# Performance work log

Measured on AMD Instinct MI355X. Metric: run time of the kernel, lower is better.

Reference implementation:

```python
import jax, jax.numpy as jnp
import numpy as np
import math

EPS = 1e-12


def _cmul(ar, ai, br, bi):
    return ar * br - ai * bi, ar * bi + ai * br


def _wilson_seed(x):
    # x: (B, 4, L, L) -> conj of canonical Wilson-line path, (B, L, L) re/im
    ux_r, ux_i, uy_r, uy_i = x[:, 0], x[:, 1], x[:, 2], x[:, 3]
    B, L, _ = ux_r.shape
    dt = x.dtype

    def step(c, u):
        cr, ci = c
        ur, ui = u
        nr, ni = _cmul(cr, ci, ur, ui)
        return (nr, ni), (nr, ni)

    # cumulative complex product along x at y=0
    init_r = jnp.ones((B,), dt)
    init_i = jnp.zeros((B,), dt)
    xs = (ux_r[:, :-1, 0].T, ux_i[:, :-1, 0].T)  # (L-1, B)
    _, (axr, axi) = jax.lax.scan(step, (init_r, init_i), xs)
    x_axis_r = jnp.concatenate([init_r[None], axr], 0).T  # (B, L)
    x_axis_i = jnp.concatenate([init_i[None], axi], 0).T

    # cumulative complex product along y, vectorized over x
    ys = (jnp.moveaxis(uy_r[:, :, :-1], 2, 0), jnp.moveaxis(uy_i[:, :, :-1], 2, 0))  # (L-1, B, L)
    _, (pr, pi_) = jax.lax.scan(step, (x_axis_r, x_axis_i), ys)
    path_r = jnp.moveaxis(jnp.concatenate([x_axis_r[None], pr], 0), 0, 2)  # (B, L, L)
    path_i = jnp.moveaxis(jnp.concatenate([x_axis_i[None], pi_], 0), 0, 2)
    return path_r, -path_i  # conjugate


def _wrap(t):
    return (t + math.pi) % (2.0 * math.pi) - math.pi


def _initial_features(x):
    seed_r, seed_i = _wilson_seed(x)
    ax = jnp.arctan2(x[:, 1], x[:, 0])
    ay = jnp.arctan2(x[:, 3], x[:, 2])
    plaq = _wrap(ax + jnp.roll(ay, -1, axis=1) - jnp.roll(ax, -1, axis=2) - ay)
    pc = jnp.cos(plaq)
    pavg = (pc + jnp.roll(pc, 1, 1) + jnp.roll(pc, -1, 1)
            + jnp.roll(pc, 1, 2) + jnp.roll(pc, -1, 2)) / 5.0
    scalars = jnp.stack([jnp.ones_like(pc), pc, pavg], axis=1)  # (B, 3, L, L)
    return seed_r[:, None] * scalars, seed_i[:, None] * scalars


def _transport_fwd(fr, fi, x, mu):
    lr, li = (x[:, 0], x[:, 1]) if mu == 0 else (x[:, 2], x[:, 3])
    sr = jnp.roll(fr, -1, axis=mu + 2)
    si = jnp.roll(fi, -1, axis=mu + 2)
    return _cmul(lr[:, None], li[:, None], sr, si)


def _transport_bwd(fr, fi, x, mu):
    lr, li = (x[:, 0], x[:, 1]) if mu == 0 else (x[:, 2], x[:, 3])
    cr = jnp.roll(lr, 1, axis=mu + 1)
    ci = jnp.roll(-li, 1, axis=mu + 1)
    sr = jnp.roll(fr, 1, axis=mu + 2)
    si = jnp.roll(fi, 1, axis=mu + 2)
    return _cmul(cr[:, None], ci[:, None], sr, si)


def _lconv(fr, fi, x, center, fwd_w, bwd_w):
    out_r = jnp.einsum('oi,bixy->boxy', center, fr)
    out_i = jnp.einsum('oi,bixy->boxy', center, fi)
    for mu in range(2):
        fr2, fi2 = _transport_fwd(fr, fi, x, mu)
        br2, bi2 = _transport_bwd(fr, fi, x, mu)
        out_r = out_r + jnp.einsum('oi,bixy->boxy', fwd_w[mu], fr2) \
                      + jnp.einsum('oi,bixy->boxy', bwd_w[mu], br2)
        out_i = out_i + jnp.einsum('oi,bixy->boxy', fwd_w[mu], fi2) \
                      + jnp.einsum('oi,bixy->boxy', bwd_w[mu], bi2)
    return out_r, out_i


def _modrelu(fr, fi, bias):
    mag = jnp.sqrt(fr * fr + fi * fi + EPS)
    act = jax.nn.relu(mag + bias[None, :, None, None])
    scale = act / jnp.maximum(mag, EPS)
    return fr * scale, fi * scale


def setup_inputs() -> dict:
    key = jax.random.key(0)
    ks = jax.random.split(key, 11)
    B, L, H, O = 64, 128, 16, 8
    s = 0.1
    return {
        'x': jax.random.normal(ks[0], (B, 4, L, L), jnp.float32),
        'center1': s * jax.random.normal(ks[1], (H, 3), jnp.float32),
        'fwd_w1': s * jax.random.normal(ks[2], (2, H, 3), jnp.float32),
        'bwd_w1': s * jax.random.normal(ks[3], (2, H, 3), jnp.float32),
        'bias1': jnp.zeros((H,), jnp.float32),
        'center2': s * jax.random.normal(ks[4], (O, H), jnp.float32),
        'fwd_w2': s * jax.random.normal(ks[5], (2, O, H), jnp.float32),
        'bwd_w2': s * jax.random.normal(ks[6], (2, O, H), jnp.float32),
        'bias2': jnp.zeros((O,), jnp.float32),
        'ro_weight': s * jax.random.normal(ks[7], (O,), jnp.float32),
        'ro_bias': jnp.zeros((1,), jnp.float32),
    }


def reference(x, center1, fwd_w1, bwd_w1, bias1, center2, fwd_w2, bwd_w2, bias2, ro_weight, ro_bias):
    fr, fi = _initial_features(x)
    fr, fi = _lconv(fr, fi, x, center1, fwd_w1, bwd_w1)
    fr, fi = _modrelu(fr, fi, bias1)
    fr, fi = _lconv(fr, fi, x, center2, fwd_w2, bwd_w2)
    fr, fi = _modrelu(fr, fi, bias2)
    inv = fr * fr + fi * fi
    return jnp.einsum('c,bcxy->bxy', ro_weight, inv)[:, None] + ro_bias.reshape(1, 1, 1, 1)
```

## Files before the change

kernel.cpp:

```cpp
#include <hip/hip_runtime.h>
#include <math.h>

#define LQ   128
#define BQ   64
#define LL   (LQ*LQ)
#define H1   16
#define O2   8
#define TILE 16
#define NTHR 512
#define NWAVE 8
#define RPW  2
#define REG  18
#define NPTS (REG*REG)
#define NPTS_PAD 336
#define NGRP 21
#define PCR  22
#define PCN  (PCR*PCR)
#define LKR  23
#define LKN  (LKR*LKR)

typedef float f2 __attribute__((ext_vector_type(2)));
using bf8 = __attribute__((ext_vector_type(8))) short;
using f4  = __attribute__((ext_vector_type(4))) float;

__device__ __forceinline__ int wrapi(int v) { return v & (LQ - 1); }

__device__ __forceinline__ unsigned cvt_pk_bf16(float lo, float hi) {
    unsigned r;
    asm("v_cvt_pk_bf16_f32 %0, %1, %2" : "=v"(r) : "v"(lo), "v"(hi));
    return r;
}

#define WS_WF ((size_t)2 * BQ * LL)

__global__ __launch_bounds__(256)
void k_scan(const float* __restrict__ x,
            const float* __restrict__ c1, const float* __restrict__ fw1,
            const float* __restrict__ bw1,
            const float* __restrict__ c2, const float* __restrict__ fw2,
            const float* __restrict__ bw2, float* __restrict__ ws) {
    int blk = blockIdx.x;
    if (blk == BQ * 8) {
        int tid = threadIdx.x;
        uint4* wf = (uint4*)(ws + WS_WF);
        if (tid < 64) {
            int kc = tid >> 4, h = tid & 15;
            unsigned dw[4];
            float v[8];
#pragma unroll
            for (int j = 0; j < 8; ++j) {
                int k = (kc & 1) * 8 + j;
                float val = 0.f;
                if (k < 15) {
                    int q = k / 3, c = k - q * 3;
                    const float* src = (q == 0) ? c1 : (q == 1) ? fw1
                                     : (q == 2) ? bw1 : (q == 3) ? (fw1 + 48)
                                     : (bw1 + 48);
                    val = src[h * 3 + c];
                }
                v[j] = val;
            }
#pragma unroll
            for (int d = 0; d < 4; ++d) dw[d] = cvt_pk_bf16(v[2*d], v[2*d+1]);
            uint4 u = {dw[0], dw[1], dw[2], dw[3]};
            wf[tid] = u;
        } else {
            int idx = tid - 64;
            int pq = idx >> 6, lane = idx & 63;
            int kc = lane >> 4, h = lane & 15, half = kc >> 1;
            const float* wsrc = half
                ? ((pq == 0) ? fw2 : (pq == 1) ? (fw2 + O2 * H1) : (const float*)0)
                : ((pq == 0) ? c2  : (pq == 1) ? bw2 : (bw2 + O2 * H1));
            unsigned dw[4] = {0u, 0u, 0u, 0u};
            int wrow = half ? (h - 8) : h;
            bool valid = half ? (h >= 8 && wsrc != 0) : (h < 8);
            if (valid) {
                const float* wp2 = wsrc + wrow * H1 + (kc & 1) * 8;
#pragma unroll
                for (int d = 0; d < 4; ++d)
                    dw[d] = cvt_pk_bf16(wp2[2*d], wp2[2*d+1]);
            }
            uint4 u = {dw[0], dw[1], dw[2], dw[3]};
            wf[64 + idx] = u;
        }
        return;
    }
    int b = blk >> 3, rq = blk & 7;
    int l = threadIdx.x & 63, w = threadIdx.x >> 6;
    const float* x0 = x + (size_t)b * 4 * LL;
    const float* x1 = x0 + LL;

    float ur0 = x0[(2 * l) * LQ],     ui0 = x1[(2 * l) * LQ];
    float ur1 = x0[(2 * l + 1) * LQ], ui1 = x1[(2 * l + 1) * LQ];
    float pr = ur0 * ur1 - ui0 * ui1;
    float pi = ur0 * ui1 + ui0 * ur1;
    for (int d = 1; d < 64; d <<= 1) {
        float qr = __shfl_up(pr, d, 64);
        float qi = __shfl_up(pi, d, 64);
        if (l >= d) {
            float nr = qr * pr - qi * pi;
            float ni = qr * pi + qi * pr;
            pr = nr; pi = ni;
        }
    }
    float er = __shfl_up(pr, 1, 64);
    float ei = __shfl_up(pi, 1, 64);
    if (l == 0) { er = 1.f; ei = 0.f; }
    float e1r = er * ur0 - ei * ui0;
    float e1i = er * ui0 + ei * ur0;

    const float* yrp = x + (size_t)(b * 4 + 2) * LL;
    const float* yip = yrp + LL;
    float4* seed4 = (float4*)ws;

    for (int k = 0; k < 4; ++k) {
        int i = rq * 16 + w * 4 + k;
        float cxr = __shfl((i & 1) ? e1r : er, i >> 1, 64);
        float cxi = __shfl((i & 1) ? e1i : ei, i >> 1, 64);
        const float* yr = yrp + (size_t)i * LQ;
        const float* yi = yip + (size_t)i * LQ;
        float vr0 = yr[2 * l],     vi0 = yi[2 * l];
        float vr1 = yr[2 * l + 1], vi1 = yi[2 * l + 1];
        float sr = vr0 * vr1 - vi0 * vi1;
        float si = vr0 * vi1 + vi0 * vr1;
        for (int d = 1; d < 64; d <<= 1) {
            float qr = __shfl_up(sr, d, 64);
            float qi = __shfl_up(si, d, 64);
            if (l >= d) {
                float nr = qr * sr - qi * si;
                float ni = qr * si + qi * sr;
                sr = nr; si = ni;
            }
        }
        float gr = __shfl_up(sr, 1, 64);
        float gi = __shfl_up(si, 1, 64);
        if (l == 0) { gr = 1.f; gi = 0.f; }
        float s0r = cxr * gr - cxi * gi;
        float s0i = cxr * gi + cxi * gr;
        float s1r = s0r * vr0 - s0i * vi0;
        float s1i = s0r * vi0 + s0i * vr0;
        seed4[((size_t)b * LL + (size_t)i * LQ) / 2 + l] =
            make_float4(s0r, -s0i, s1r, -s1i);
    }
}

__global__ __launch_bounds__(NTHR, 6)
void k_main(const float* __restrict__ x,
            const float* __restrict__ b1, const float* __restrict__ b2,
            const float* __restrict__ ro, const float* __restrict__ rob,
            const float* __restrict__ ws, float* __restrict__ out) {
    __shared__ __align__(16) unsigned s_f1[NPTS_PAD * 32];
    __shared__ f2 s_ux[LKN];
    __shared__ f2 s_uy[LKN];
    __shared__ float s_pc[PCN];
    int tid = threadIdx.x;
    int b = blockIdx.z, i0 = blockIdx.y * TILE, j0 = blockIdx.x * TILE;
    const float* x0 = x + (size_t)b * 4 * LL;
    const float* x1 = x0 + LL;
    const float* x2 = x0 + 2 * LL;
    const float* x3 = x0 + 3 * LL;
    const float2* seed = (const float2*)ws + (size_t)b * LL;
    const uint4* wf = (const uint4*)(ws + WS_WF);

    int lane = tid & 63, w = tid >> 6;
    int kc = lane >> 4, h = lane & 15, half = kc >> 1;

    bool z1 = true;
#pragma unroll
    for (int hh = 0; hh < H1; ++hh) z1 = z1 && (b1[hh] == 0.f);
    bool z2 = true;
#pragma unroll
    for (int oo = 0; oo < O2; ++oo) z2 = z2 && (b2[oo] == 0.f);

    bf8 a1;
    { uint4 u = wf[lane]; __builtin_memcpy(&a1, &u, 16); }
    bf8 afr[3];
#pragma unroll
    for (int pq = 0; pq < 3; ++pq) {
        uint4 u = wf[64 + pq * 64 + lane];
        __builtin_memcpy(&afr[pq], &u, 16);
    }

    for (int p = tid; p < LKN; p += NTHR) {
        int ri = p / LKR, rj = p - ri * LKR;
        int gi = wrapi(i0 - 3 + ri), gj = wrapi(j0 - 3 + rj);
        int idx = gi * LQ + gj;
        s_ux[p] = (f2){x0[idx], x1[idx]};
        s_uy[p] = (f2){x2[idx], x3[idx]};
    }
    __syncthreads();

    for (int p = tid; p < PCN; p += NTHR) {
        int ri = p / PCR, rj = p - ri * PCR;
        int lb = ri * LKR + rj;
        f2 u1 = s_ux[lb];
        f2 u2 = s_uy[lb + LKR];
        f2 u3 = s_ux[lb + 1];
        f2 u4 = s_uy[lb];
        float ar = u1.x * u2.x - u1.y * u2.y, ai = u1.x * u2.y + u1.y * u2.x;
        float br = ar * u3.x + ai * u3.y,     bi = -ar * u3.y + ai * u3.x;
        float zr = br * u4.x + bi * u4.y,     zi = -br * u4.y + bi * u4.x;
        s_pc[p] = zr * __frsqrt_rn(fmaf(zr, zr, zi * zi) + 1e-30f);
    }
    __syncthreads();

    for (int p = tid; p < NPTS_PAD; p += NTHR) {
        int rot = p & 7;
        unsigned* dst = &s_f1[p * 32];
        if (p < NPTS) {
            int ri = p / REG, rj = p - ri * REG;
            int lb = (ri + 2) * LKR + (rj + 2);
            int cb = (ri + 2) * PCR + (rj + 2);

            int gi0 = wrapi(i0 - 1 + ri), gim = wrapi(i0 - 2 + ri), gip = wrapi(i0 + ri);
            int gj0 = wrapi(j0 - 1 + rj), gjm = wrapi(j0 - 2 + rj), gjp = wrapi(j0 + rj);
            float2 SC  = seed[gi0 * LQ + gj0];
            float2 SXP = seed[gip * LQ + gj0];
            float2 SXM = seed[gim * LQ + gj0];
            float2 SYP = seed[gi0 * LQ + gjp];
            float2 SYM = seed[gi0 * LQ + gjm];

            f2 lx = s_ux[lb], ly = s_uy[lb];
            f2 mx = s_ux[lb - LKR], my = s_uy[lb - 1];
            float tr[5], ti[5], tc[5], tv[5];
            tr[0] = SC.x;                          ti[0] = SC.y;
            tr[1] = lx.x * SXP.x - lx.y * SXP.y;   ti[1] = lx.x * SXP.y + lx.y * SXP.x;
            tr[2] = mx.x * SXM.x + mx.y * SXM.y;   ti[2] = mx.x * SXM.y - mx.y * SXM.x;
            tr[3] = ly.x * SYP.x - ly.y * SYP.y;   ti[3] = ly.x * SYP.y + ly.y * SYP.x;
            tr[4] = my.x * SYM.x + my.y * SYM.y;   ti[4] = my.x * SYM.y - my.y * SYM.x;

            float p00 = s_pc[cb];
            float pP0 = s_pc[cb + PCR],     pM0 = s_pc[cb - PCR];
            float p0P = s_pc[cb + 1],       p0M = s_pc[cb - 1];
            float pP20 = s_pc[cb + 2*PCR],  pM20 = s_pc[cb - 2*PCR];
            float p0P2 = s_pc[cb + 2],      p0M2 = s_pc[cb - 2];
            float pPP = s_pc[cb + PCR + 1], pPM = s_pc[cb + PCR - 1];
            float pMP = s_pc[cb - PCR + 1], pMM = s_pc[cb - PCR - 1];
            tc[0] = p00; tc[1] = pP0; tc[2] = pM0; tc[3] = p0P; tc[4] = p0M;
            tv[0] = (p00 + pP0 + pM0 + p0P + p0M) * 0.2f;
            tv[1] = (pP0 + pP20 + p00 + pPP + pPM) * 0.2f;
            tv[2] = (pM0 + p00 + pM20 + pMP + pMM) * 0.2f;
            tv[3] = (p0P + pPP + pMP + p0P2 + p00) * 0.2f;
            tv[4] = (p0M + pPM + pMM + p00 + p0M2) * 0.2f;

            float Fr[16], Fi[16];
#pragma unroll
            for (int q = 0; q < 5; ++q) {
                Fr[3*q]   = tr[q];         Fi[3*q]   = ti[q];
                Fr[3*q+1] = tc[q]*tr[q];   Fi[3*q+1] = tc[q]*ti[q];
                Fr[3*q+2] = tv[q]*tr[q];   Fi[3*q+2] = tv[q]*ti[q];
            }
            Fr[15] = 0.f; Fi[15] = 0.f;
            unsigned hr[8], hi_[8], lr[8], li_[8];
#pragma unroll
            for (int d = 0; d < 8; ++d) {
                hr[d]  = cvt_pk_bf16(Fr[2*d], Fr[2*d+1]);
                hi_[d] = cvt_pk_bf16(Fi[2*d], Fi[2*d+1]);
                float r0 = Fr[2*d]   - __uint_as_float(hr[d] << 16);
                float r1 = Fr[2*d+1] - __uint_as_float(hr[d] & 0xFFFF0000u);
                float q0 = Fi[2*d]   - __uint_as_float(hi_[d] << 16);
                float q1 = Fi[2*d+1] - __uint_as_float(hi_[d] & 0xFFFF0000u);
                lr[d]  = cvt_pk_bf16(r0, r1);
                li_[d] = cvt_pk_bf16(q0, q1);
            }
            uint4 vs0 = {hr[0], hr[1], hr[2], hr[3]};
            uint4 vs1 = {hr[4], hr[5], hr[6], hr[7]};
            uint4 vs2 = {hi_[0], hi_[1], hi_[2], hi_[3]};
            uint4 vs3 = {hi_[4], hi_[5], hi_[6], hi_[7]};
            uint4 vs4 = {lr[0], lr[1], lr[2], lr[3]};
            uint4 vs5 = {lr[4], lr[5], lr[6], lr[7]};
            uint4 vs6 = {li_[0], li_[1], li_[2], li_[3]};
            uint4 vs7 = {li_[4], li_[5], li_[6], li_[7]};
            *(uint4*)&dst[((0 + rot) & 7) * 4] = vs0;
            *(uint4*)&dst[((1 + rot) & 7) * 4] = vs1;
            *(uint4*)&dst[((2 + rot) & 7) * 4] = vs2;
            *(uint4*)&dst[((3 + rot) & 7) * 4] = vs3;
            *(uint4*)&dst[((4 + rot) & 7) * 4] = vs4;
            *(uint4*)&dst[((5 + rot) & 7) * 4] = vs5;
            *(uint4*)&dst[((6 + rot) & 7) * 4] = vs6;
            *(uint4*)&dst[((7 + rot) & 7) * 4] = vs7;
        } else {
            uint4 z = {0u, 0u, 0u, 0u};
#pragma unroll
            for (int s = 0; s < 8; ++s) *(uint4*)&dst[s * 4] = z;
        }
    }
    __syncthreads();

    for (int g = w; g < NGRP; g += NWAVE) {
        int P = g * 16 + h;
        int rot = P & 7;
        unsigned* bb = &s_f1[P * 32];
        int sr = (kc < 2) ? kc : (kc + 2);
        uint4 ur = *(const uint4*)&bb[((sr + rot) & 7) * 4];
        uint4 ui = *(const uint4*)&bb[((sr + 2 + rot) & 7) * 4];
        bf8 br, bi;
        __builtin_memcpy(&br, &ur, 16);
        __builtin_memcpy(&bi, &ui, 16);
        f4 zc = {0.f, 0.f, 0.f, 0.f};
        f4 Dr = __builtin_amdgcn_mfma_f32_16x16x32_bf16(a1, br, zc, 0, 0, 0);
        f4 Di = __builtin_amdgcn_mfma_f32_16x16x32_bf16(a1, bi, zc, 0, 0, 0);
        if (P < NPTS) {
            if (!z1) {
#pragma unroll
                for (int r = 0; r < 4; ++r) {
                    float q2 = Dr[r]*Dr[r] + Di[r]*Di[r] + 1e-12f;
                    float s = fmaxf(fmaf(b1[4*kc + r], __frsqrt_rn(q2), 1.f), 0.f);
                    Dr[r] *= s; Di[r] *= s;
                }
            }
            unsigned pr0 = cvt_pk_bf16(Dr[0], Dr[1]);
            unsigned pr1 = cvt_pk_bf16(Dr[2], Dr[3]);
            unsigned pi0 = cvt_pk_bf16(Di[0], Di[1]);
            unsigned pi1 = cvt_pk_bf16(Di[2], Di[3]);
            int base = P * 32 + ((kc & 1) << 1);
            int ar = base + ((((kc >> 1) + rot) & 7) << 2);
            int ai = base + ((((kc >> 1) + 2 + rot) & 7) << 2);
            *(uint2*)&s_f1[ar] = make_uint2(pr0, pr1);
            *(uint2*)&s_f1[ai] = make_uint2(pi0, pi1);
        }
    }
    __syncthreads();

    float4 ro_lo = *(const float4*)ro;
    float4 ro_hi = *(const float4*)(ro + 4);
    float4 b2_lo = *(const float4*)b2;
    float4 b2_hi = *(const float4*)(b2 + 4);
    float4 zf4 = make_float4(0.f, 0.f, 0.f, 0.f);
    float4 rv = (kc == 0) ? ro_lo : ((kc == 1) ? ro_hi : zf4);
    float4 bv = (kc == 0) ? b2_lo : ((kc == 1) ? b2_hi : zf4);
    float rob0 = rob[0];

    int dpl[3];
    dpl[0] = half ? REG : 0;
    dpl[1] = half ? 1 : -REG;
    dpl[2] = -1;

#pragma unroll
    for (int g = 0; g < RPW; ++g) {
        int row = w * RPW + g;
        int posc = (row + 1) * REG + (h + 1);
        int lb2 = (row + 3) * LKR + (h + 3);
        f2 lx = s_ux[lb2], ly = s_uy[lb2];
        f2 mx = s_ux[lb2 - LKR], my = s_uy[lb2 - 1];

        float Lr[3], Li[3];
        Lr[0] = half ? lx.x : 1.f;   Li[0] = half ? lx.y : 0.f;
        Lr[1] = half ? ly.x : mx.x;  Li[1] = half ? ly.y : -mx.y;
        Lr[2] = half ? 0.f : my.x;   Li[2] = half ? 0.f : -my.y;

        f2 a2r01 = {0.f, 0.f}, a2r23 = {0.f, 0.f};
        f2 a2i01 = {0.f, 0.f}, a2i23 = {0.f, 0.f};
#pragma unroll
        for (int pq = 0; pq < 3; ++pq) {
            int posc2 = posc + dpl[pq];
            int rot2 = posc2 & 7;
            int bb = posc2 * 32;
            uint4 ur = *(const uint4*)&s_f1[bb + ((((kc & 1) + rot2) & 7) << 2)];
            uint4 ui = *(const uint4*)&s_f1[bb + ((((kc & 1) + 2 + rot2) & 7) << 2)];
            bf8 br, bi;
            __builtin_memcpy(&br, &ur, 16);
            __builtin_memcpy(&bi, &ui, 16);
            f4 zc = {0.f, 0.f, 0.f, 0.f};
            f4 sr = __builtin_amdgcn_mfma_f32_16x16x32_bf16(afr[pq], br, zc, 0, 0, 0);
            f4 si = __builtin_amdgcn_mfma_f32_16x16x32_bf16(afr[pq], bi, zc, 0, 0, 0);
            f2 sr01 = {sr[0], sr[1]}, sr23 = {sr[2], sr[3]};
            f2 si01 = {si[0], si[1]}, si23 = {si[2], si[3]};
            a2r01 += Lr[pq] * sr01 - Li[pq] * si01;
            a2r23 += Lr[pq] * sr23 - Li[pq] * si23;
            a2i01 += Lr[pq] * si01 + Li[pq] * sr01;
            a2i23 += Lr[pq] * si23 + Li[pq] * sr23;
        }

        float ar_[4], ai_[4];
        ar_[0] = a2r01.x; ar_[1] = a2r01.y; ar_[2] = a2r23.x; ar_[3] = a2r23.y;
        ai_[0] = a2i01.x; ai_[1] = a2i01.y; ai_[2] = a2i23.x; ai_[3] = a2i23.y;
#pragma unroll
        for (int c = 0; c < 4; ++c) {
            ar_[c] += __shfl_xor(ar_[c], 32, 64);
            ai_[c] += __shfl_xor(ai_[c], 32, 64);
        }

        float q4[4];
#pragma unroll
        for (int c = 0; c < 4; ++c)
            q4[c] = ar_[c] * ar_[c] + ai_[c] * ai_[c];
        float res;
        if (z2) {
            res = rv.x * q4[0] + rv.y * q4[1] + rv.z * q4[2] + rv.w * q4[3];
        } else {
            float bvv[4] = {bv.x, bv.y, bv.z, bv.w};
            float rvv[4] = {rv.x, rv.y, rv.z, rv.w};
            res = 0.f;
#pragma unroll
            for (int r = 0; r < 4; ++r) {
                float qq = q4[r];
                float s = fmaxf(fmaf(bvv[r], __frsqrt_rn(qq + 1e-12f), 1.f), 0.f);
                res = fmaf(rvv[r], s * s * qq, res);
            }
        }
        res += __shfl_xor(res, 16, 64);
        if (kc == 0)
            out[(size_t)b * LL + (size_t)(i0 + row) * LQ + (j0 + h)] = res + rob0;
    }
}

extern "C" void kernel_launch(void* const* d_in, const int* in_sizes, int n_in,
                              void* d_out, int out_size, void* d_ws, size_t ws_size,
                              hipStream_t stream) {
    const float* x   = (const float*)d_in[0];
    const float* c1  = (const float*)d_in[1];
    const float* fw1 = (const float*)d_in[2];
    const float* bw1 = (const float*)d_in[3];
    const float* b1  = (const float*)d_in[4];
    const float* c2  = (const float*)d_in[5];
    const float* fw2 = (const float*)d_in[6];
    const float* bw2 = (const float*)d_in[7];
    const float* b2  = (const float*)d_in[8];
    const float* ro  = (const float*)d_in[9];
    const float* rob = (const float*)d_in[10];
    float* out = (float*)d_out;
    float* ws  = (float*)d_ws;

    k_scan<<<BQ * 8 + 1, 256, 0, stream>>>(x, c1, fw1, bw1, c2, fw2, bw2, ws);
    dim3 grid(LQ / TILE, LQ / TILE, BQ);
    k_main<<<grid, NTHR, 0, stream>>>(x, b1, b2, ro, rob, ws, out);
}
```

Baseline: 129.0 us.

## Replace split-bf16 layer-1 features with per-point scaled fp16 MFMA

The layer-1 input features were stored as hi/lo bf16 pairs (a split emulating higher precision) and multiplied with two MFMAs per K-chunk. They are now normalised by a per-point max magnitude, stored once as fp16 and multiplied with f16 MFMA, and the scale is reapplied from a new shared array afterwards. This halves the shared-memory feature buffer and the conversion work, and raises the occupancy hint from 6 to 8 blocks. The trade is fp16's 11-bit mantissa in place of the roughly 16-bit hi+lo bf16 split, which could loosen accuracy.

```diff
diff --git a/kernel.cpp b/kernel.cpp
--- a/kernel.cpp
+++ b/kernel.cpp
@@ -21,6 +21,7 @@
 
 typedef float f2 __attribute__((ext_vector_type(2)));
 using bf8 = __attribute__((ext_vector_type(8))) short;
+using hf8 = __attribute__((ext_vector_type(8))) _Float16;
 using f4  = __attribute__((ext_vector_type(4))) float;
 
 __device__ __forceinline__ int wrapi(int v) { return v & (LQ - 1); }
@@ -28,6 +29,12 @@
 __device__ __forceinline__ unsigned cvt_pk_bf16(float lo, float hi) {
     unsigned r;
     asm("v_cvt_pk_bf16_f32 %0, %1, %2" : "=v"(r) : "v"(lo), "v"(hi));
+    return r;
+}
+__device__ __forceinline__ unsigned cvt_pk_f16(float lo, float hi) {
+    auto h2 = __builtin_amdgcn_cvt_pkrtz(lo, hi);
+    unsigned r;
+    __builtin_memcpy(&r, &h2, 4);
     return r;
 }
 
@@ -49,7 +56,7 @@
             float v[8];
 #pragma unroll
             for (int j = 0; j < 8; ++j) {
-                int k = (kc & 1) * 8 + j;
+                int k = kc * 8 + j;
                 float val = 0.f;
                 if (k < 15) {
                     int q = k / 3, c = k - q * 3;
@@ -61,7 +68,7 @@
                 v[j] = val;
             }
 #pragma unroll
-            for (int d = 0; d < 4; ++d) dw[d] = cvt_pk_bf16(v[2*d], v[2*d+1]);
+            for (int d = 0; d < 4; ++d) dw[d] = cvt_pk_f16(v[2*d], v[2*d+1]);
             uint4 u = {dw[0], dw[1], dw[2], dw[3]};
             wf[tid] = u;
         } else {
@@ -144,15 +151,16 @@
     }
 }
 
-__global__ __launch_bounds__(NTHR, 6)
+__global__ __launch_bounds__(NTHR, 8)
 void k_main(const float* __restrict__ x,
             const float* __restrict__ b1, const float* __restrict__ b2,
             const float* __restrict__ ro, const float* __restrict__ rob,
             const float* __restrict__ ws, float* __restrict__ out) {
-    __shared__ __align__(16) unsigned s_f1[NPTS_PAD * 32];
+    __shared__ __align__(16) unsigned s_f1[NPTS_PAD * 16];
     __shared__ f2 s_ux[LKN];
     __shared__ f2 s_uy[LKN];
     __shared__ float s_pc[PCN];
+    __shared__ float s_m[NPTS_PAD];
     int tid = threadIdx.x;
     int b = blockIdx.z, i0 = blockIdx.y * TILE, j0 = blockIdx.x * TILE;
     const float* x0 = x + (size_t)b * 4 * LL;
@@ -172,7 +180,7 @@
 #pragma unroll
     for (int oo = 0; oo < O2; ++oo) z2 = z2 && (b2[oo] == 0.f);
 
-    bf8 a1;
+    hf8 a1;
     { uint4 u = wf[lane]; __builtin_memcpy(&a1, &u, 16); }
     bf8 afr[3];
 #pragma unroll
@@ -205,8 +213,8 @@
     __syncthreads();
 
     for (int p = tid; p < NPTS_PAD; p += NTHR) {
-        int rot = p & 7;
-        unsigned* dst = &s_f1[p * 32];
+        int rot = (p >> 1) & 3;
+        unsigned* dst = &s_f1[p * 16];
         if (p < NPTS) {
             int ri = p / REG, rj = p - ri * REG;
             int lb = (ri + 2) * LKR + (rj + 2);
@@ -243,79 +251,75 @@
             tv[3] = (p0P + pPP + pMP + p0P2 + p00) * 0.2f;
             tv[4] = (p0M + pPM + pMM + p00 + p0M2) * 0.2f;
 
+            float m = 1e-30f;
+#pragma unroll
+            for (int q = 0; q < 5; ++q)
+                m = fmaxf(m, fmaxf(fabsf(tr[q]), fabsf(ti[q])));
+            float s = __frcp_rn(m);
+
             float Fr[16], Fi[16];
 #pragma unroll
             for (int q = 0; q < 5; ++q) {
-                Fr[3*q]   = tr[q];         Fi[3*q]   = ti[q];
-                Fr[3*q+1] = tc[q]*tr[q];   Fi[3*q+1] = tc[q]*ti[q];
-                Fr[3*q+2] = tv[q]*tr[q];   Fi[3*q+2] = tv[q]*ti[q];
+                float trq = tr[q] * s, tiq = ti[q] * s;
+                Fr[3*q]   = trq;          Fi[3*q]   = tiq;
+                Fr[3*q+1] = tc[q]*trq;    Fi[3*q+1] = tc[q]*tiq;
+                Fr[3*q+2] = tv[q]*trq;    Fi[3*q+2] = tv[q]*tiq;
             }
             Fr[15] = 0.f; Fi[15] = 0.f;
-            unsigned hr[8], hi_[8], lr[8], li_[8];
+            unsigned hr[8], hi_[8];
 #pragma unroll
             for (int d = 0; d < 8; ++d) {
-                hr[d]  = cvt_pk_bf16(Fr[2*d], Fr[2*d+1]);
-                hi_[d] = cvt_pk_bf16(Fi[2*d], Fi[2*d+1]);
-                float r0 = Fr[2*d]   - __uint_as_float(hr[d] << 16);
-                float r1 = Fr[2*d+1] - __uint_as_float(hr[d] & 0xFFFF0000u);
-                float q0 = Fi[2*d]   - __uint_as_float(hi_[d] << 16);
-                float q1 = Fi[2*d+1] - __uint_as_float(hi_[d] & 0xFFFF0000u);
-                lr[d]  = cvt_pk_bf16(r0, r1);
-                li_[d] = cvt_pk_bf16(q0, q1);
+                hr[d]  = cvt_pk_f16(Fr[2*d], Fr[2*d+1]);
+                hi_[d] = cvt_pk_f16(Fi[2*d], Fi[2*d+1]);
             }
             uint4 vs0 = {hr[0], hr[1], hr[2], hr[3]};
             uint4 vs1 = {hr[4], hr[5], hr[6], hr[7]};
             uint4 vs2 = {hi_[0], hi_[1], hi_[2], hi_[3]};
             uint4 vs3 = {hi_[4], hi_[5], hi_[6], hi_[7]};
-            uint4 vs4 = {lr[0], lr[1], lr[2], lr[3]};
-            uint4 vs5 = {lr[4], lr[5], lr[6], lr[7]};
-            uint4 vs6 = {li_[0], li_[1], li_[2], li_[3]};
-            uint4 vs7 = {li_[4], li_[5], li_[6], li_[7]};
-            *(uint4*)&dst[((0 + rot) & 7) * 4] = vs0;
-            *(uint4*)&dst[((1 + rot) & 7) * 4] = vs1;
-            *(uint4*)&dst[((2 + rot) & 7) * 4] = vs2;
-            *(uint4*)&dst[((3 + rot) & 7) * 4] = vs3;
-            *(uint4*)&dst[((4 + rot) & 7) * 4] = vs4;
-            *(uint4*)&dst[((5 + rot) & 7) * 4] = vs5;
-            *(uint4*)&dst[((6 + rot) & 7) * 4] = vs6;
-            *(uint4*)&dst[((7 + rot) & 7) * 4] = vs7;
+            *(uint4*)&dst[((0 + rot) & 3) * 4] = vs0;
+            *(uint4*)&dst[((1 + rot) & 3) * 4] = vs1;
+            *(uint4*)&dst[((2 + rot) & 3) * 4] = vs2;
+            *(uint4*)&dst[((3 + rot) & 3) * 4] = vs3;
+            s_m[p] = m;
         } else {
             uint4 z = {0u, 0u, 0u, 0u};
 #pragma unroll
-            for (int s = 0; s < 8; ++s) *(uint4*)&dst[s * 4] = z;
+            for (int sl = 0; sl < 4; ++sl) *(uint4*)&dst[sl * 4] = z;
+            s_m[p] = 0.f;
         }
     }
     __syncthreads();
 
     for (int g = w; g < NGRP; g += NWAVE) {
         int P = g * 16 + h;
-        int rot = P & 7;
-        unsigned* bb = &s_f1[P * 32];
-        int sr = (kc < 2) ? kc : (kc + 2);
-        uint4 ur = *(const uint4*)&bb[((sr + rot) & 7) * 4];
-        uint4 ui = *(const uint4*)&bb[((sr + 2 + rot) & 7) * 4];
-        bf8 br, bi;
+        int rot = (P >> 1) & 3;
+        unsigned* bb = &s_f1[P * 16];
+        uint4 ur = *(const uint4*)&bb[((kc + rot) & 3) * 4];
+        uint4 ui = *(const uint4*)&bb[(((kc ^ 2) + rot) & 3) * 4];
+        hf8 br, bi;
         __builtin_memcpy(&br, &ur, 16);
         __builtin_memcpy(&bi, &ui, 16);
         f4 zc = {0.f, 0.f, 0.f, 0.f};
-        f4 Dr = __builtin_amdgcn_mfma_f32_16x16x32_bf16(a1, br, zc, 0, 0, 0);
-        f4 Di = __builtin_amdgcn_mfma_f32_16x16x32_bf16(a1, bi, zc, 0, 0, 0);
+        f4 Dr = __builtin_amdgcn_mfma_f32_16x16x32_f16(a1, br, zc, 0, 0, 0);
+        f4 Di = __builtin_amdgcn_mfma_f32_16x16x32_f16(a1, bi, zc, 0, 0, 0);
         if (P < NPTS) {
+            float mm = s_m[P];
+            Dr *= mm; Di *= mm;
             if (!z1) {
 #pragma unroll
                 for (int r = 0; r < 4; ++r) {
                     float q2 = Dr[r]*Dr[r] + Di[r]*Di[r] + 1e-12f;
-                    float s = fmaxf(fmaf(b1[4*kc + r], __frsqrt_rn(q2), 1.f), 0.f);
-                    Dr[r] *= s; Di[r] *= s;
+                    float sb = fmaxf(fmaf(b1[4*kc + r], __frsqrt_rn(q2), 1.f), 0.f);
+                    Dr[r] *= sb; Di[r] *= sb;
                 }
             }
             unsigned pr0 = cvt_pk_bf16(Dr[0], Dr[1]);
             unsigned pr1 = cvt_pk_bf16(Dr[2], Dr[3]);
             unsigned pi0 = cvt_pk_bf16(Di[0], Di[1]);
             unsigned pi1 = cvt_pk_bf16(Di[2], Di[3]);
-            int base = P * 32 + ((kc & 1) << 1);
-            int ar = base + ((((kc >> 1) + rot) & 7) << 2);
-            int ai = base + ((((kc >> 1) + 2 + rot) & 7) << 2);
+            int base = P * 16 + ((kc & 1) << 1);
+            int ar = base + ((((kc >> 1) + rot) & 3) << 2);
+            int ai = base + ((((kc >> 1) + 2 + rot) & 3) << 2);
             *(uint2*)&s_f1[ar] = make_uint2(pr0, pr1);
             *(uint2*)&s_f1[ai] = make_uint2(pi0, pi1);
         }
@@ -354,10 +358,10 @@
 #pragma unroll
         for (int pq = 0; pq < 3; ++pq) {
             int posc2 = posc + dpl[pq];
-            int rot2 = posc2 & 7;
-            int bb = posc2 * 32;
-            uint4 ur = *(const uint4*)&s_f1[bb + ((((kc & 1) + rot2) & 7) << 2)];
-            uint4 ui = *(const uint4*)&s_f1[bb + ((((kc & 1) + 2 + rot2) & 7) << 2)];
+            int rot2 = (posc2 >> 1) & 3;
+            int bbb = posc2 * 16;
+            uint4 ur = *(const uint4*)&s_f1[bbb + ((((kc & 1) + rot2) & 3) << 2)];
+            uint4 ui = *(const uint4*)&s_f1[bbb + ((((kc & 1) + 2 + rot2) & 3) << 2)];
             bf8 br, bi;
             __builtin_memcpy(&br, &ur, 16);
             __builtin_memcpy(&bi, &ui, 16);
@@ -395,8 +399,8 @@
 #pragma unroll
             for (int r = 0; r < 4; ++r) {
                 float qq = q4[r];
-                float s = fmaxf(fmaf(bvv[r], __frsqrt_rn(qq + 1e-12f), 1.f), 0.f);
-                res = fmaf(rvv[r], s * s * qq, res);
+                float sb = fmaxf(fmaf(bvv[r], __frsqrt_rn(qq + 1e-12f), 1.f), 0.f);
+                res = fmaf(rvv[r], sb * sb * qq, res);
             }
         }
         res += __shfl_xor(res, 16, 64);
```

Result: faster. 123.6 us (median of 2 runs) (-4.2%).
